# Performance work log

Measured on AMD Instinct MI355X. Metric: run time of the kernel, lower is better.

Reference implementation:

```python
import jax, jax.numpy as jnp
import numpy as np

N_NODES = 50000
N_EDGES = 800000
NODE_DIM = 64
EDGE_DIM = 32
OUT_FEATS = 64


def setup_inputs() -> dict:
    key = jax.random.key(0)
    k1, k2, k3, k4, k5, k6, k7 = jax.random.split(key, 7)
    node_features = jax.random.normal(k1, (N_NODES, NODE_DIM), dtype=jnp.float32)
    edge_features = jax.random.normal(k2, (N_EDGES, EDGE_DIM), dtype=jnp.float32)
    src = jax.random.randint(k3, (N_EDGES,), 0, N_NODES, dtype=jnp.int32)
    dst = jax.random.randint(k4, (N_EDGES,), 0, N_NODES, dtype=jnp.int32)
    in_dim = 2 * NODE_DIM + EDGE_DIM  # concat([e_ft, h_src, h_dst])
    w_group = jax.random.normal(k5, (in_dim,), dtype=jnp.float32) * 0.05
    w_srcattn = jax.random.normal(k6, (NODE_DIM + EDGE_DIM,), dtype=jnp.float32) * 0.05
    w_lin = jax.random.normal(k7, (in_dim, OUT_FEATS), dtype=jnp.float32) * 0.05
    return {"node_features": node_features, "edge_features": edge_features,
            "src": src, "dst": dst,
            "w_group": w_group, "w_srcattn": w_srcattn, "w_lin": w_lin}


def _segment_softmax(scores, seg, num_segments):
    # numerically-stable softmax of per-edge scalar scores within each segment
    m = jax.ops.segment_max(scores, seg, num_segments=num_segments)
    e = jnp.exp(scores - m[seg])
    s = jax.ops.segment_sum(e, seg, num_segments=num_segments)
    return e / s[seg]


def reference(node_features, edge_features, src, dst, w_group, w_srcattn, w_lin):
    h = node_features              # [N, node_dim]
    e_ft = edge_features           # [E, edge_dim]
    h_src = h[src]                 # [E, node_dim]
    h_dst = h[dst]                 # [E, node_dim]

    # --- group_apply_edges(group_by='src'): edge attention over out-edges of each src ---
    z2 = jnp.concatenate([e_ft, h_src, h_dst], axis=1)      # [E, edge_dim + 2*node_dim]
    a = z2 @ w_group                                        # [E]
    gamma = _segment_softmax(a, src, N_NODES)               # softmax over edges sharing src
    e_weighted = gamma[:, None] * e_ft                      # [E, edge_dim]

    # --- gnn_msg: msg = concat([h_src, e_weighted]) ---
    msg = jnp.concatenate([h_src, e_weighted], axis=1)      # [E, node_dim + edge_dim]

    # --- gnn_reduce: attention softmax over mailbox (edges sharing dst), weighted sum ---
    s = msg @ w_srcattn                                     # [E]
    alpha = _segment_softmax(s, dst, N_NODES)
    accum = jax.ops.segment_sum(alpha[:, None] * msg, dst, num_segments=N_NODES)  # [N, node_dim+edge_dim]

    # --- node_update: linear(concat([h, accum])) + relu ---
    h_cat = jnp.concatenate([h, accum], axis=1)             # [N, 2*node_dim + edge_dim]
    out = jax.nn.relu(h_cat @ w_lin)                        # [N, out_feats]
    return out
```

## Files before the change

### kernel.cpp

```cpp
#include <hip/hip_runtime.h>

#define NN 50000
#define NE 800000
#define NEB 3125
#define NHB 3125
#define NTILES 3125

typedef __attribute__((ext_vector_type(8))) short bf16x8;
typedef __attribute__((ext_vector_type(4))) short s16x4;
typedef __attribute__((ext_vector_type(4))) float f32x4;
typedef __attribute__((ext_vector_type(4))) int   i32x4;

static __device__ __forceinline__ short f2bf(float f) {
    unsigned int u = __float_as_uint(f);
    u += 0x7FFFu + ((u >> 16) & 1u);
    return (short)(u >> 16);
}
static __device__ __forceinline__ float bf2f(short b) {
    return __uint_as_float(((unsigned)(unsigned short)b) << 16);
}

__global__ __launch_bounds__(256) void k_pre(
    const float* __restrict__ h, const int* __restrict__ dst,
    const float* __restrict__ wg, const float* __restrict__ wa,
    int* __restrict__ cnt, float* __restrict__ p1, float* __restrict__ pd,
    float* __restrict__ dpf, short* __restrict__ hb)
{
    int tid = threadIdx.x;
    if (blockIdx.x < NEB) {
        int e = blockIdx.x * 256 + tid;
        if (e < NE) atomicAdd(&cnt[dst[e]], 1);
        return;
    }
    __shared__ float4 ls[16], ld[16], lt[16];
    if (tid < 16)      ls[tid]      = ((const float4*)wg)[8 + tid];
    else if (tid < 32) ld[tid - 16] = ((const float4*)wg)[8 + tid];
    else if (tid < 48) lt[tid - 32] = ((const float4*)wa)[tid - 32];
    __syncthreads();
    int n = (blockIdx.x - NEB) * 16 + (tid >> 4);
    if (n >= NN) return;
    int l16 = tid & 15;
    float4 v = ((const float4*)(h + (size_t)n * 64))[l16];
    s16x4 hv;
    hv[0] = f2bf(v.x); hv[1] = f2bf(v.y); hv[2] = f2bf(v.z); hv[3] = f2bf(v.w);
    *(s16x4*)(hb + (size_t)n * 160 + l16 * 4) = hv;
    float4 w1 = ls[l16], w2 = ld[l16], w3 = lt[l16];
    float s1 = v.x*w1.x + v.y*w1.y + v.z*w1.z + v.w*w1.w;
    float s2 = v.x*w2.x + v.y*w2.y + v.z*w2.z + v.w*w2.w;
    float s3 = v.x*w3.x + v.y*w3.y + v.z*w3.z + v.w*w3.w;
    #pragma unroll
    for (int m = 8; m; m >>= 1) {
        s1 += __shfl_xor(s1, m);
        s2 += __shfl_xor(s2, m);
        s3 += __shfl_xor(s3, m);
    }
    if (l16 == 0) { p1[n] = s1; pd[n] = s2; dpf[2 * n + 1] = s3; }
}

__global__ __launch_bounds__(256) void k_assign(
    const int* __restrict__ cnt, int* __restrict__ off, int* __restrict__ cursor,
    int* __restrict__ gtotal)
{
    int n = blockIdx.x * 256 + threadIdx.x;
    int lane = threadIdx.x & 63;
    int c = (n < NN) ? cnt[n] : 0;
    int pre = c;
    #pragma unroll
    for (int d = 1; d < 64; d <<= 1) {
        int v = __shfl_up(pre, d);
        if (lane >= d) pre += v;
    }
    int base = 0;
    if (lane == 63) base = atomicAdd(gtotal, pre);
    base = __shfl(base, 63);
    if (n < NN) { int b = base + pre - c; off[n] = b; cursor[n] = b; }
}

__global__ __launch_bounds__(256) void k_edge(
    const float* __restrict__ ef, const int* __restrict__ src,
    const int* __restrict__ dst, const float* __restrict__ wg,
    const float* __restrict__ wa, const float* __restrict__ p1,
    const float* __restrict__ pd, float* __restrict__ dpf,
    int* __restrict__ cursor, i32x4* __restrict__ recA)
{
    __shared__ float4 lwe[8], lae[8];
    int tid = threadIdx.x;
    if (tid < 8)       lwe[tid]     = ((const float4*)wg)[tid];
    else if (tid < 16) lae[tid - 8] = ((const float4*)wa)[tid - 8 + 16];
    __syncthreads();
    int e = blockIdx.x * 256 + tid;
    if (e >= NE) return;
    int s = src[e], d = dst[e];
    float p1v = p1[s], pdv = pd[d];
    const float4* e4 = (const float4*)(ef + (size_t)e * 32);
    float a = 0.f, u = 0.f;
    #pragma unroll
    for (int q = 0; q < 8; ++q) {
        float4 v = e4[q], w = lwe[q], w2 = lae[q];
        a += v.x*w.x  + v.y*w.y  + v.z*w.z  + v.w*w.w;
        u += v.x*w2.x + v.y*w2.y + v.z*w2.z + v.w*w2.w;
    }
    float ev = __expf(a + p1v + pdv);
    atomicAdd(&dpf[2 * s], ev);
    int pos = atomicAdd(&cursor[d], 1);
    recA[pos] = (i32x4){s, e, __float_as_int(ev), __float_as_int(u)};
}

__global__ __launch_bounds__(256) void k_reduce(
    const float* __restrict__ ef, const int* __restrict__ off,
    const int* __restrict__ cursor, const float2* __restrict__ dp,
    const i32x4* __restrict__ recA, short* __restrict__ hb)
{
    int n = blockIdx.x * 4 + (threadIdx.x >> 6);
    if (n >= NN) return;
    int lane = threadIdx.x & 63;
    bool up = lane >= 32;
    int l5 = lane & 31;
    int base = off[n];
    int deg = cursor[n] - base;
    const i32x4* rp = recA + base;
    float acch = 0.f, acce = 0.f, den = 0.f;
    int j = 0;
    for (; j + 8 <= deg; j += 8) {
        i32x4 r[8];
        #pragma unroll
        for (int t = 0; t < 8; ++t) r[t] = rp[j + t];
        float2 dv[8]; float hv[8];
        #pragma unroll
        for (int t = 0; t < 8; ++t) {
            dv[t] = dp[r[t][0]];
            hv[t] = bf2f(hb[(size_t)(unsigned)r[t][0] * 160 + lane]);
        }
        float efv[4];
        #pragma unroll
        for (int t = 0; t < 4; ++t) {
            int ee = up ? r[2*t+1][1] : r[2*t][1];
            efv[t] = ef[((unsigned)ee << 5) + l5];
        }
        float g[8], s[8];
        #pragma unroll
        for (int t = 0; t < 8; ++t) {
            g[t] = __int_as_float(r[t][2]) * __builtin_amdgcn_rcpf(dv[t].x);
            s[t] = __expf(dv[t].y + g[t] * __int_as_float(r[t][3]));
            den  += s[t];
            acch += s[t] * hv[t];
        }
        #pragma unroll
        for (int t = 0; t < 4; ++t) {
            float w = up ? s[2*t+1]*g[2*t+1] : s[2*t]*g[2*t];
            acce += w * efv[t];
        }
    }
    if (j + 4 <= deg) {
        i32x4 r[4];
        #pragma unroll
        for (int t = 0; t < 4; ++t) r[t] = rp[j + t];
        float2 dv[4]; float hv[4];
        #pragma unroll
        for (int t = 0; t < 4; ++t) {
            dv[t] = dp[r[t][0]];
            hv[t] = bf2f(hb[(size_t)(unsigned)r[t][0] * 160 + lane]);
        }
        float efv[2];
        #pragma unroll
        for (int t = 0; t < 2; ++t) {
            int ee = up ? r[2*t+1][1] : r[2*t][1];
            efv[t] = ef[((unsigned)ee << 5) + l5];
        }
        float g[4], s[4];
        #pragma unroll
        for (int t = 0; t < 4; ++t) {
            g[t] = __int_as_float(r[t][2]) * __builtin_amdgcn_rcpf(dv[t].x);
            s[t] = __expf(dv[t].y + g[t] * __int_as_float(r[t][3]));
            den  += s[t];
            acch += s[t] * hv[t];
        }
        #pragma unroll
        for (int t = 0; t < 2; ++t) {
            float w = up ? s[2*t+1]*g[2*t+1] : s[2*t]*g[2*t];
            acce += w * efv[t];
        }
        j += 4;
    }
    for (; j < deg; ++j) {
        i32x4 r = rp[j];
        float2 dt = dp[r[0]];
        float g = __int_as_float(r[2]) * __builtin_amdgcn_rcpf(dt.x);
        float sx = __expf(dt.y + g * __int_as_float(r[3]));
        den += sx;
        acch += sx * bf2f(hb[(size_t)(unsigned)r[0] * 160 + lane]);
        if (!up) acce += sx * g * ef[((unsigned)r[1] << 5) + l5];
    }
    acce += __shfl_xor(acce, 32);
    float inv = (deg > 0) ? __builtin_amdgcn_rcpf(den) : 0.f;
    size_t hbase = (size_t)n * 160;
    hb[hbase + 64 + lane] = f2bf(acch * inv);
    if (!up) hb[hbase + 128 + l5] = f2bf(acce * inv);
}

__global__ __launch_bounds__(256) void k_node_update(
    const short* __restrict__ hb, const float* __restrict__ wl_g,
    float* __restrict__ out)
{
    int lane = threadIdx.x & 63;
    int col  = lane & 15;
    int quad = lane >> 4;
    int tile = blockIdx.x * 4 + (threadIdx.x >> 6);
    if (tile >= NTILES) return;

    bf16x8 bfr[5][4];
    #pragma unroll
    for (int kc = 0; kc < 5; ++kc)
        #pragma unroll
        for (int nt = 0; nt < 4; ++nt) {
            #pragma unroll
            for (int j = 0; j < 8; ++j) {
                int k = kc * 32 + quad * 8 + j;
                bfr[kc][nt][j] = f2bf(wl_g[k * 64 + nt * 16 + col]);
            }
        }

    int n = tile * 16 + col;
    f32x4 acc[4];
    #pragma unroll
    for (int nt = 0; nt < 4; ++nt) acc[nt] = (f32x4){0.f, 0.f, 0.f, 0.f};

    const short* hrow = hb + (size_t)n * 160 + quad * 8;
    #pragma unroll
    for (int kc = 0; kc < 5; ++kc) {
        bf16x8 af = *(const bf16x8*)(hrow + kc * 32);
        #pragma unroll
        for (int nt = 0; nt < 4; ++nt)
            acc[nt] = __builtin_amdgcn_mfma_f32_16x16x32_bf16(
                af, bfr[kc][nt], acc[nt], 0, 0, 0);
    }

    #pragma unroll
    for (int nt = 0; nt < 4; ++nt) {
        #pragma unroll
        for (int r = 0; r < 4; ++r) {
            int node = tile * 16 + quad * 4 + r;
            out[(size_t)node * 64 + nt * 16 + col] = fmaxf(acc[nt][r], 0.f);
        }
    }
}

extern "C" void kernel_launch(void* const* d_in, const int* in_sizes, int n_in,
                              void* d_out, int out_size, void* d_ws, size_t ws_size,
                              hipStream_t stream)
{
    const float* h   = (const float*)d_in[0];
    const float* ef  = (const float*)d_in[1];
    const int*   src = (const int*)d_in[2];
    const int*   dst = (const int*)d_in[3];
    const float* wg  = (const float*)d_in[4];
    const float* wa  = (const float*)d_in[5];
    const float* wl  = (const float*)d_in[6];
    float* out = (float*)d_out;

    float*  ws     = (float*)d_ws;
    float*  dpf    = ws;
    int*    cnt    = (int*)(ws + 2 * NN);
    int*    gtotal = (int*)(ws + 3 * NN);
    int*    off    = (int*)(ws + 3 * NN + 16);
    int*    cursor = (int*)(ws + 4 * NN + 16);
    float*  p1     = ws + 5 * NN + 16;
    float*  pd     = ws + 6 * NN + 16;
    i32x4*  recA   = (i32x4*)(ws + 7 * NN + 16);
    short*  hb     = (short*)(ws + 7 * NN + 16 + 4 * NE);

    hipMemsetAsync(d_ws, 0, (size_t)(3 * NN + 16) * sizeof(float), stream);

    k_pre<<<NEB + NHB, 256, 0, stream>>>(h, dst, wg, wa, cnt, p1, pd, dpf, hb);
    k_assign<<<(NN + 255) / 256, 256, 0, stream>>>(cnt, off, cursor, gtotal);
    k_edge<<<NEB, 256, 0, stream>>>(ef, src, dst, wg, wa, p1, pd, dpf,
                                    cursor, recA);
    k_reduce<<<(NN + 3) / 4, 256, 0, stream>>>(ef, off, cursor,
                                               (const float2*)dpf, recA, hb);
    k_node_update<<<782, 256, 0, stream>>>(hb, wl, out);
}
```

Baseline: 360.8 us.

## Precompute per-edge rank in counting pass; preconvert weights to bf16 transposed

```diff
diff --git a/kernel.cpp b/kernel.cpp
--- a/kernel.cpp
+++ b/kernel.cpp
@@ -23,13 +23,14 @@
 __global__ __launch_bounds__(256) void k_pre(
     const float* __restrict__ h, const int* __restrict__ dst,
     const float* __restrict__ wg, const float* __restrict__ wa,
-    int* __restrict__ cnt, float* __restrict__ p1, float* __restrict__ pd,
-    float* __restrict__ dpf, short* __restrict__ hb)
+    int* __restrict__ cnt, int* __restrict__ rank,
+    float* __restrict__ p1, float* __restrict__ pd, float* __restrict__ dpf,
+    short* __restrict__ hb)
 {
     int tid = threadIdx.x;
     if (blockIdx.x < NEB) {
         int e = blockIdx.x * 256 + tid;
-        if (e < NE) atomicAdd(&cnt[dst[e]], 1);
+        if (e < NE) rank[e] = atomicAdd(&cnt[dst[e]], 1);
         return;
     }
     __shared__ float4 ls[16], ld[16], lt[16];
@@ -58,9 +59,15 @@
 }
 
 __global__ __launch_bounds__(256) void k_assign(
-    const int* __restrict__ cnt, int* __restrict__ off, int* __restrict__ cursor,
-    int* __restrict__ gtotal)
-{
+    const int* __restrict__ cnt, int* __restrict__ off, int* __restrict__ gtotal,
+    const float* __restrict__ wl, short* __restrict__ wlbT)
+{
+    if (blockIdx.x >= 196) {
+        int idx = (blockIdx.x - 196) * 256 + threadIdx.x;
+        int k = idx >> 6, nn = idx & 63;
+        wlbT[nn * 160 + k] = f2bf(wl[idx]);
+        return;
+    }
     int n = blockIdx.x * 256 + threadIdx.x;
     int lane = threadIdx.x & 63;
     int c = (n < NN) ? cnt[n] : 0;
@@ -73,15 +80,16 @@
     int base = 0;
     if (lane == 63) base = atomicAdd(gtotal, pre);
     base = __shfl(base, 63);
-    if (n < NN) { int b = base + pre - c; off[n] = b; cursor[n] = b; }
+    if (n < NN) off[n] = base + pre - c;
 }
 
 __global__ __launch_bounds__(256) void k_edge(
     const float* __restrict__ ef, const int* __restrict__ src,
-    const int* __restrict__ dst, const float* __restrict__ wg,
-    const float* __restrict__ wa, const float* __restrict__ p1,
-    const float* __restrict__ pd, float* __restrict__ dpf,
-    int* __restrict__ cursor, i32x4* __restrict__ recA)
+    const int* __restrict__ dst, const int* __restrict__ rank,
+    const float* __restrict__ wg, const float* __restrict__ wa,
+    const float* __restrict__ p1, const float* __restrict__ pd,
+    float* __restrict__ dpf, const int* __restrict__ off,
+    i32x4* __restrict__ recA)
 {
     __shared__ float4 lwe[8], lae[8];
     int tid = threadIdx.x;
@@ -90,8 +98,9 @@
     __syncthreads();
     int e = blockIdx.x * 256 + tid;
     if (e >= NE) return;
-    int s = src[e], d = dst[e];
+    int s = src[e], d = dst[e], rk = rank[e];
     float p1v = p1[s], pdv = pd[d];
+    int pos = off[d] + rk;
     const float4* e4 = (const float4*)(ef + (size_t)e * 32);
     float a = 0.f, u = 0.f;
     #pragma unroll
@@ -102,13 +111,12 @@
     }
     float ev = __expf(a + p1v + pdv);
     atomicAdd(&dpf[2 * s], ev);
-    int pos = atomicAdd(&cursor[d], 1);
     recA[pos] = (i32x4){s, e, __float_as_int(ev), __float_as_int(u)};
 }
 
 __global__ __launch_bounds__(256) void k_reduce(
-    const float* __restrict__ ef, const int* __restrict__ off,
-    const int* __restrict__ cursor, const float2* __restrict__ dp,
+    const float* __restrict__ ef, const int* __restrict__ cnt,
+    const int* __restrict__ off, const float2* __restrict__ dp,
     const i32x4* __restrict__ recA, short* __restrict__ hb)
 {
     int n = blockIdx.x * 4 + (threadIdx.x >> 6);
@@ -116,8 +124,7 @@
     int lane = threadIdx.x & 63;
     bool up = lane >= 32;
     int l5 = lane & 31;
-    int base = off[n];
-    int deg = cursor[n] - base;
+    int deg = cnt[n], base = off[n];
     const i32x4* rp = recA + base;
     float acch = 0.f, acce = 0.f, den = 0.f;
     int j = 0;
@@ -199,48 +206,47 @@
 }
 
 __global__ __launch_bounds__(256) void k_node_update(
-    const short* __restrict__ hb, const float* __restrict__ wl_g,
+    const short* __restrict__ hb, const short* __restrict__ wlbT,
     float* __restrict__ out)
 {
     int lane = threadIdx.x & 63;
     int col  = lane & 15;
     int quad = lane >> 4;
-    int tile = blockIdx.x * 4 + (threadIdx.x >> 6);
-    if (tile >= NTILES) return;
+    int wid  = blockIdx.x * 4 + (threadIdx.x >> 6);
+    int nwaves = gridDim.x * 4;
 
     bf16x8 bfr[5][4];
     #pragma unroll
-    for (int kc = 0; kc < 5; ++kc)
+    for (int nt = 0; nt < 4; ++nt) {
+        const short* bp = wlbT + (size_t)(nt * 16 + col) * 160 + quad * 8;
+        #pragma unroll
+        for (int kc = 0; kc < 5; ++kc)
+            bfr[kc][nt] = *(const bf16x8*)(bp + kc * 32);
+    }
+
+    for (int tile = wid; tile < NTILES; tile += nwaves) {
+        int n = tile * 16 + col;
+        f32x4 acc[4];
+        #pragma unroll
+        for (int nt = 0; nt < 4; ++nt) acc[nt] = (f32x4){0.f, 0.f, 0.f, 0.f};
+
+        const short* hrow = hb + (size_t)n * 160 + quad * 8;
+        #pragma unroll
+        for (int kc = 0; kc < 5; ++kc) {
+            bf16x8 af = *(const bf16x8*)(hrow + kc * 32);
+            #pragma unroll
+            for (int nt = 0; nt < 4; ++nt)
+                acc[nt] = __builtin_amdgcn_mfma_f32_16x16x32_bf16(
+                    af, bfr[kc][nt], acc[nt], 0, 0, 0);
+        }
+
         #pragma unroll
         for (int nt = 0; nt < 4; ++nt) {
             #pragma unroll
-            for (int j = 0; j < 8; ++j) {
-                int k = kc * 32 + quad * 8 + j;
-                bfr[kc][nt][j] = f2bf(wl_g[k * 64 + nt * 16 + col]);
+            for (int r = 0; r < 4; ++r) {
+                int node = tile * 16 + quad * 4 + r;
+                out[(size_t)node * 64 + nt * 16 + col] = fmaxf(acc[nt][r], 0.f);
             }
-        }
-
-    int n = tile * 16 + col;
-    f32x4 acc[4];
-    #pragma unroll
-    for (int nt = 0; nt < 4; ++nt) acc[nt] = (f32x4){0.f, 0.f, 0.f, 0.f};
-
-    const short* hrow = hb + (size_t)n * 160 + quad * 8;
-    #pragma unroll
-    for (int kc = 0; kc < 5; ++kc) {
-        bf16x8 af = *(const bf16x8*)(hrow + kc * 32);
-        #pragma unroll
-        for (int nt = 0; nt < 4; ++nt)
-            acc[nt] = __builtin_amdgcn_mfma_f32_16x16x32_bf16(
-                af, bfr[kc][nt], acc[nt], 0, 0, 0);
-    }
-
-    #pragma unroll
-    for (int nt = 0; nt < 4; ++nt) {
-        #pragma unroll
-        for (int r = 0; r < 4; ++r) {
-            int node = tile * 16 + quad * 4 + r;
-            out[(size_t)node * 64 + nt * 16 + col] = fmaxf(acc[nt][r], 0.f);
         }
     }
 }
@@ -263,19 +269,21 @@
     int*    cnt    = (int*)(ws + 2 * NN);
     int*    gtotal = (int*)(ws + 3 * NN);
     int*    off    = (int*)(ws + 3 * NN + 16);
-    int*    cursor = (int*)(ws + 4 * NN + 16);
-    float*  p1     = ws + 5 * NN + 16;
-    float*  pd     = ws + 6 * NN + 16;
-    i32x4*  recA   = (i32x4*)(ws + 7 * NN + 16);
-    short*  hb     = (short*)(ws + 7 * NN + 16 + 4 * NE);
+    float*  p1     = ws + 4 * NN + 16;
+    float*  pd     = ws + 5 * NN + 16;
+    int*    rank   = (int*)(ws + 6 * NN + 16);
+    short*  wlbT   = (short*)(ws + 6 * NN + 16 + NE);
+    i32x4*  recA   = (i32x4*)(ws + 6 * NN + 16 + NE + 5120);
+    short*  hb     = (short*)(ws + 6 * NN + 16 + 5 * NE + 5120);
 
     hipMemsetAsync(d_ws, 0, (size_t)(3 * NN + 16) * sizeof(float), stream);
 
-    k_pre<<<NEB + NHB, 256, 0, stream>>>(h, dst, wg, wa, cnt, p1, pd, dpf, hb);
-    k_assign<<<(NN + 255) / 256, 256, 0, stream>>>(cnt, off, cursor, gtotal);
-    k_edge<<<NEB, 256, 0, stream>>>(ef, src, dst, wg, wa, p1, pd, dpf,
-                                    cursor, recA);
-    k_reduce<<<(NN + 3) / 4, 256, 0, stream>>>(ef, off, cursor,
+    k_pre<<<NEB + NHB, 256, 0, stream>>>(h, dst, wg, wa, cnt, rank, p1, pd,
+                                         dpf, hb);
+    k_assign<<<236, 256, 0, stream>>>(cnt, off, gtotal, wl, wlbT);
+    k_edge<<<NEB, 256, 0, stream>>>(ef, src, dst, rank, wg, wa, p1, pd, dpf,
+                                    off, recA);
+    k_reduce<<<(NN + 3) / 4, 256, 0, stream>>>(ef, cnt, off,
                                                (const float2*)dpf, recA, hb);
-    k_node_update<<<782, 256, 0, stream>>>(hb, wl, out);
-}
+    k_node_update<<<391, 256, 0, stream>>>(hb, wlbT, out);
+}
```

After: 339.9 us. -5.8%, faster.
